# Kernel optimization log

Hardware: AMD Instinct MI355X
Metric: run time of the kernel (lower is better)

## Reference

```python
import jax, jax.numpy as jnp
import numpy as np


def _tet_geometry(vertices, indices, tet_density):
    """Gather 4 corners per tet, compute area (|det|/6), min edge length, alpha."""
    v = vertices[indices]                      # [T,4,3]
    v0, v1, v2, v3 = v[:, 0], v[:, 1], v[:, 2], v[:, 3]
    # --- tet area: |det([v1-v0, v2-v0, v3-v0])| / 6 ---
    e1, e2, e3 = v1 - v0, v2 - v0, v3 - v0     # [T,3] each
    det = (e1[:, 0] * (e2[:, 1] * e3[:, 2] - e2[:, 2] * e3[:, 1])
           - e1[:, 1] * (e2[:, 0] * e3[:, 2] - e2[:, 2] * e3[:, 0])
           + e1[:, 2] * (e2[:, 0] * e3[:, 1] - e2[:, 1] * e3[:, 0]))
    tet_area = jnp.abs(det) / 6.0              # [T]
    # --- edge lengths of all 6 edges, take min (mode='min') ---
    edge_sq = jnp.stack([
        jnp.sum((v0 - v1) ** 2, axis=1),
        jnp.sum((v0 - v2) ** 2, axis=1),
        jnp.sum((v0 - v3) ** 2, axis=1),
        jnp.sum((v1 - v2) ** 2, axis=1),
        jnp.sum((v1 - v3) ** 2, axis=1),
        jnp.sum((v2 - v3) ** 2, axis=1),
    ], axis=0)                                 # [6,T]
    el = jnp.sqrt(jnp.min(edge_sq, axis=0))    # [T]
    tet_alpha = 1.0 - jnp.exp(-tet_density * el)
    return tet_area, tet_alpha


def _vert_density(tet_density, indices, num_verts):
    # torch scatter_reduce_ 'amax' with zero-initialized dest and include_self=True
    # == segment_max over all 4 corner slots, clamped below at 0.
    flat_idx = indices.reshape(-1)                         # [4T]
    src = jnp.repeat(tet_density, 4)                       # [4T], matches row-major flatten
    vmax = jax.ops.segment_max(src, flat_idx, num_segments=num_verts)
    return jnp.maximum(vmax, jnp.zeros((), vmax.dtype))    # untouched verts -> 0


def setup_inputs() -> dict:
    key = jax.random.key(0)
    k1, k2, k3 = jax.random.split(key, 3)
    V, T = 1_000_000, 4_000_000
    vertices = jax.random.normal(k1, (V, 3), dtype=jnp.float32)
    indices = jax.random.randint(k2, (T, 4), 0, V, dtype=jnp.int32)
    tet_density = jax.random.uniform(k3, (T,), dtype=jnp.float32)
    return {"vertices": vertices, "indices": indices, "tet_density": tet_density}


def reference(vertices, indices, tet_density):
    tet_area, tet_alpha = _tet_geometry(vertices, indices, tet_density)
    vert_density = _vert_density(tet_density, indices, vertices.shape[0])
    return tet_area, tet_alpha, vert_density
```

## Files before the change

### kernel.cpp

```cpp
#include <hip/hip_runtime.h>

typedef int nt_int4 __attribute__((ext_vector_type(4)));

#define NB     256
#define VSHIFT 12
#define BMASK  ((1 << VSHIFT) - 1)
#define BCAP   65536
#define RT     2
#define NR     4

__global__ __launch_bounds__(256) void setup_kernel(uint4* __restrict__ vd4, int n4,
                                                    unsigned* __restrict__ gcnt,
                                                    const float* __restrict__ verts,
                                                    float4* __restrict__ verts4, int V) {
    int i = blockIdx.x * blockDim.x + threadIdx.x;
    if (i < n4) vd4[i] = make_uint4(0u, 0u, 0u, 0u);
    if (gcnt && i < NB) gcnt[i] = 0u;
    if (verts4 && i < V) {
        const float* p = verts + (size_t)i * 3;
        verts4[i] = make_float4(p[0], p[1], p[2], 0.f);
    }
}

__global__ __launch_bounds__(256) void fused_geom_bin_kernel(
    const float4* __restrict__ verts4,
    const int4*  __restrict__ idx4,
    const float* __restrict__ dens,
    float* __restrict__ out_area,
    float* __restrict__ out_alpha,
    uint2*       __restrict__ pairs,
    unsigned*    __restrict__ gcnt,
    unsigned*    __restrict__ vd,
    int T)
{
    __shared__ unsigned s_cnt[NB];
    __shared__ unsigned s_run[NB];
    __shared__ unsigned s_roff[NB];
    __shared__ unsigned s_wc[NB];
    __shared__ unsigned s_wsum[4];
    __shared__ uint2    stage[256 * RT * 4];

    int tid  = threadIdx.x;
    int lane = tid & 63;
    int wid  = tid >> 6;
    int base = blockIdx.x * (256 * RT * NR);

    s_cnt[tid] = 0u;
    __syncthreads();
    for (int k = 0; k < RT * NR; ++k) {
        int i = base + k * 256 + tid;
        if (i < T) {
            int4 q = idx4[i];
            atomicAdd(&s_cnt[(unsigned)q.x >> VSHIFT], 1u);
            atomicAdd(&s_cnt[(unsigned)q.y >> VSHIFT], 1u);
            atomicAdd(&s_cnt[(unsigned)q.z >> VSHIFT], 1u);
            atomicAdd(&s_cnt[(unsigned)q.w >> VSHIFT], 1u);
        }
    }
    __syncthreads();

    s_run[tid] = atomicAdd(&gcnt[tid], s_cnt[tid]);
    __syncthreads();

    int4  q[RT], qn[RT];
    float dd[RT], ddn[RT];
    bool  vl[RT], vln[RT];
    float4 pv[RT][4];

#pragma unroll
    for (int k = 0; k < RT; ++k) {
        int i = base + k * 256 + tid;
        vl[k] = (i < T);
        if (vl[k]) { q[k] = idx4[i]; dd[k] = dens[i]; }
    }
#pragma unroll
    for (int k = 0; k < RT; ++k) if (vl[k]) {
        pv[k][0] = verts4[q[k].x];
        pv[k][1] = verts4[q[k].y];
        pv[k][2] = verts4[q[k].z];
        pv[k][3] = verts4[q[k].w];
    }

    for (int r = 0; r < NR; ++r) {
        if (r + 1 < NR) {
#pragma unroll
            for (int k = 0; k < RT; ++k) {
                int i = base + ((r + 1) * RT + k) * 256 + tid;
                vln[k] = (i < T);
                if (vln[k]) { qn[k] = idx4[i]; ddn[k] = dens[i]; }
            }
        }

#pragma unroll
        for (int k = 0; k < RT; ++k) if (vl[k]) {
            int i = base + (r * RT + k) * 256 + tid;
            float4 v0 = pv[k][0], v1 = pv[k][1], v2 = pv[k][2], v3 = pv[k][3];

            float e1x = v1.x - v0.x, e1y = v1.y - v0.y, e1z = v1.z - v0.z;
            float e2x = v2.x - v0.x, e2y = v2.y - v0.y, e2z = v2.z - v0.z;
            float e3x = v3.x - v0.x, e3y = v3.y - v0.y, e3z = v3.z - v0.z;

            float det = e1x * (e2y * e3z - e2z * e3y)
                      - e1y * (e2x * e3z - e2z * e3x)
                      + e1z * (e2x * e3y - e2y * e3x);
            __builtin_nontemporal_store(fabsf(det) * (1.0f / 6.0f), &out_area[i]);

            float q01 = e1x * e1x + e1y * e1y + e1z * e1z;
            float q02 = e2x * e2x + e2y * e2y + e2z * e2z;
            float q03 = e3x * e3x + e3y * e3y + e3z * e3z;
            float ax, ay, az;
            ax = v1.x - v2.x; ay = v1.y - v2.y; az = v1.z - v2.z;
            float q12 = ax * ax + ay * ay + az * az;
            ax = v1.x - v3.x; ay = v1.y - v3.y; az = v1.z - v3.z;
            float q13 = ax * ax + ay * ay + az * az;
            ax = v2.x - v3.x; ay = v2.y - v3.y; az = v2.z - v3.z;
            float q23 = ax * ax + ay * ay + az * az;

            float mn = fminf(fminf(fminf(q01, q02), fminf(q03, q12)), fminf(q13, q23));
            float el = sqrtf(mn);
            __builtin_nontemporal_store(1.0f - expf(-dd[k] * el), &out_alpha[i]);
        }

        s_cnt[tid] = 0u;
        __syncthreads();
#pragma unroll
        for (int k = 0; k < RT; ++k) if (vl[k]) {
            atomicAdd(&s_cnt[(unsigned)q[k].x >> VSHIFT], 1u);
            atomicAdd(&s_cnt[(unsigned)q[k].y >> VSHIFT], 1u);
            atomicAdd(&s_cnt[(unsigned)q[k].z >> VSHIFT], 1u);
            atomicAdd(&s_cnt[(unsigned)q[k].w >> VSHIFT], 1u);
        }
        __syncthreads();

        unsigned x = s_cnt[tid];
        unsigned incl = x;
#pragma unroll
        for (int s = 1; s < 64; s <<= 1) {
            unsigned t = __shfl_up(incl, s);
            if (lane >= s) incl += t;
        }
        if (lane == 63) s_wsum[wid] = incl;
        __syncthreads();
        unsigned pre = 0;
#pragma unroll
        for (int w = 0; w < 4; ++w) pre += (w < wid) ? s_wsum[w] : 0u;
        unsigned npairs = s_wsum[0] + s_wsum[1] + s_wsum[2] + s_wsum[3];
        s_roff[tid] = pre + incl - x;
        s_wc[tid]   = 0u;
        __syncthreads();

        if (r + 1 < NR) {
#pragma unroll
            for (int k = 0; k < RT; ++k) if (vln[k]) {
                pv[k][0] = verts4[qn[k].x];
                pv[k][1] = verts4[qn[k].y];
                pv[k][2] = verts4[qn[k].z];
                pv[k][3] = verts4[qn[k].w];
            }
        }

#pragma unroll
        for (int k = 0; k < RT; ++k) if (vl[k]) {
            unsigned db = __float_as_uint(dd[k]);
            unsigned vv[4] = { (unsigned)q[k].x, (unsigned)q[k].y,
                               (unsigned)q[k].z, (unsigned)q[k].w };
#pragma unroll
            for (int j = 0; j < 4; ++j) {
                unsigned b    = vv[j] >> VSHIFT;
                unsigned slot = s_roff[b] + atomicAdd(&s_wc[b], 1u);
                stage[slot] = make_uint2(vv[j], db);
            }
        }
        __syncthreads();

        for (unsigned l = tid; l < npairs; l += 256) {
            uint2 e = stage[l];
            unsigned b  = e.x >> VSHIFT;
            unsigned rr = s_run[b] + (l - s_roff[b]);
            if (rr < BCAP) pairs[(size_t)b * BCAP + rr] = e;
            else           atomicMax(vd + e.x, e.y);
        }
        __syncthreads();

        s_run[tid] += s_cnt[tid];
#pragma unroll
        for (int k = 0; k < RT; ++k) { q[k] = qn[k]; dd[k] = ddn[k]; vl[k] = vln[k]; }
    }
}

__global__ __launch_bounds__(1024) void bucket_max_kernel(
    const uint2*    __restrict__ pairs,
    const unsigned* __restrict__ gcnt,
    unsigned*       __restrict__ vd,
    int V)
{
    __shared__ unsigned tbl[1 << VSHIFT];
    int b   = blockIdx.x;
    int tid = threadIdx.x;

    for (int j = tid; j < (1 << VSHIFT); j += 1024) tbl[j] = 0u;
    __syncthreads();

    unsigned cnt = gcnt[b];
    if (cnt > BCAP) cnt = BCAP;
    const uint2* p = pairs + (size_t)b * BCAP;
    for (unsigned i = tid; i < cnt; i += 1024) {
        uint2 e = p[i];
        atomicMax(&tbl[e.x & BMASK], e.y);
    }
    __syncthreads();

    int vbase = b << VSHIFT;
    for (int j = tid; j < (1 << VSHIFT); j += 1024) {
        int v = vbase + j;
        if (v < V) {
            unsigned cur = vd[v];
            unsigned t   = tbl[j];
            vd[v] = cur > t ? cur : t;
        }
    }
}

__global__ __launch_bounds__(256) void tet_kernel_filter(
    const float4* __restrict__ verts4,
    const int*   __restrict__ indices,
    const float* __restrict__ density,
    float* __restrict__ out_area,
    float* __restrict__ out_alpha,
    unsigned int* __restrict__ vd,
    int T)
{
    int i = blockIdx.x * blockDim.x + threadIdx.x;
    if (i >= T) return;

    nt_int4 idx = __builtin_nontemporal_load((const nt_int4*)indices + i);
    float d     = __builtin_nontemporal_load(&density[i]);
    unsigned int db = __float_as_uint(d);

    unsigned int c0 = vd[idx.x];
    unsigned int c1 = vd[idx.y];
    unsigned int c2 = vd[idx.z];
    unsigned int c3 = vd[idx.w];

    float4 v0 = verts4[idx.x];
    float4 v1 = verts4[idx.y];
    float4 v2 = verts4[idx.z];
    float4 v3 = verts4[idx.w];

    float e1x = v1.x - v0.x, e1y = v1.y - v0.y, e1z = v1.z - v0.z;
    float e2x = v2.x - v0.x, e2y = v2.y - v0.y, e2z = v2.z - v0.z;
    float e3x = v3.x - v0.x, e3y = v3.y - v0.y, e3z = v3.z - v0.z;

    float det = e1x * (e2y * e3z - e2z * e3y)
              - e1y * (e2x * e3z - e2z * e3x)
              + e1z * (e2x * e3y - e2y * e3x);
    __builtin_nontemporal_store(fabsf(det) * (1.0f / 6.0f), &out_area[i]);

    float q01 = e1x * e1x + e1y * e1y + e1z * e1z;
    float q02 = e2x * e2x + e2y * e2y + e2z * e2z;
    float q03 = e3x * e3x + e3y * e3y + e3z * e3z;
    float ax, ay, az;
    ax = v1.x - v2.x; ay = v1.y - v2.y; az = v1.z - v2.z;
    float q12 = ax * ax + ay * ay + az * az;
    ax = v1.x - v3.x; ay = v1.y - v3.y; az = v1.z - v3.z;
    float q13 = ax * ax + ay * ay + az * az;
    ax = v2.x - v3.x; ay = v2.y - v3.y; az = v2.z - v3.z;
    float q23 = ax * ax + ay * ay + az * az;

    float mn = fminf(fminf(fminf(q01, q02), fminf(q03, q12)), fminf(q13, q23));
    float el = sqrtf(mn);
    __builtin_nontemporal_store(1.0f - expf(-d * el), &out_alpha[i]);

    if (db > c0) atomicMax(vd + idx.x, db);
    if (db > c1) atomicMax(vd + idx.y, db);
    if (db > c2) atomicMax(vd + idx.z, db);
    if (db > c3) atomicMax(vd + idx.w, db);
}

__global__ __launch_bounds__(256) void tet_kernel_fb(
    const float* __restrict__ verts,
    const int4*  __restrict__ indices,
    const float* __restrict__ density,
    float* __restrict__ out_area,
    float* __restrict__ out_alpha,
    unsigned int* __restrict__ vd,
    int T)
{
    int i = blockIdx.x * blockDim.x + threadIdx.x;
    if (i >= T) return;

    int4 idx = indices[i];
    float d = density[i];

    const float* p;
    p = verts + idx.x * 3; float v0x = p[0], v0y = p[1], v0z = p[2];
    p = verts + idx.y * 3; float v1x = p[0], v1y = p[1], v1z = p[2];
    p = verts + idx.z * 3; float v2x = p[0], v2y = p[1], v2z = p[2];
    p = verts + idx.w * 3; float v3x = p[0], v3y = p[1], v3z = p[2];

    float e1x = v1x - v0x, e1y = v1y - v0y, e1z = v1z - v0z;
    float e2x = v2x - v0x, e2y = v2y - v0y, e2z = v2z - v0z;
    float e3x = v3x - v0x, e3y = v3y - v0y, e3z = v3z - v0z;

    float det = e1x * (e2y * e3z - e2z * e3y)
              - e1y * (e2x * e3z - e2z * e3x)
              + e1z * (e2x * e3y - e2y * e3x);
    out_area[i] = fabsf(det) * (1.0f / 6.0f);

    float q01 = e1x * e1x + e1y * e1y + e1z * e1z;
    float q02 = e2x * e2x + e2y * e2y + e2z * e2z;
    float q03 = e3x * e3x + e3y * e3y + e3z * e3z;
    float ax, ay, az;
    ax = v1x - v2x; ay = v1y - v2y; az = v1z - v2z;
    float q12 = ax * ax + ay * ay + az * az;
    ax = v1x - v3x; ay = v1y - v3y; az = v1z - v3z;
    float q13 = ax * ax + ay * ay + az * az;
    ax = v2x - v3x; ay = v2y - v3y; az = v2z - v3z;
    float q23 = ax * ax + ay * ay + az * az;

    float mn = fminf(fminf(fminf(q01, q02), fminf(q03, q12)), fminf(q13, q23));
    float el = sqrtf(mn);
    out_alpha[i] = 1.0f - expf(-d * el);

    unsigned int db = __float_as_uint(d);
    atomicMax(vd + idx.x, db);
    atomicMax(vd + idx.y, db);
    atomicMax(vd + idx.z, db);
    atomicMax(vd + idx.w, db);
}


extern "C" void kernel_launch(void* const* d_in, const int* in_sizes, int n_in,
                              void* d_out, int out_size, void* d_ws, size_t ws_size,
                              hipStream_t stream) {
    const float* verts   = (const float*)d_in[0];
    const int*   indices = (const int*)d_in[1];
    const float* density = (const float*)d_in[2];
    int T = in_sizes[2];
    int V = in_sizes[0] / 3;

    float* out       = (float*)d_out;
    float* out_area  = out;
    float* out_alpha = out + (size_t)T;
    unsigned int* vd = (unsigned int*)(out + 2 * (size_t)T);

    const int block = 256;
    int n4 = V / 4;

    size_t pairsB = (size_t)NB * BCAP * sizeof(uint2);
    size_t cntB   = (size_t)NB * sizeof(unsigned);
    size_t v4B    = (size_t)V * sizeof(float4);

    double mean = 4.0 * (double)T / NB;
    bool capOK = (mean + 12.0 * __builtin_sqrt(mean) <= (double)BCAP);
    bool fastOK = (V % 4 == 0) && (V <= (NB << VSHIFT)) && capOK && d_ws;

    int tetsPerBlock = block * RT * NR;
    int nbAct = (V + (1 << VSHIFT) - 1) >> VSHIFT;

    if (fastOK && ws_size >= pairsB + cntB + v4B) {
        uint2*    pairs  = (uint2*)d_ws;
        unsigned* gcnt   = (unsigned*)((char*)d_ws + pairsB);
        float4*   verts4 = (float4*)((char*)d_ws + pairsB + ((cntB + 255) & ~(size_t)255));

        int setupN = (V > n4 ? V : n4);
        setup_kernel<<<(setupN + block - 1) / block, block, 0, stream>>>(
            (uint4*)vd, n4, gcnt, verts, verts4, V);

        fused_geom_bin_kernel<<<(T + tetsPerBlock - 1) / tetsPerBlock, block, 0, stream>>>(
            verts4, (const int4*)indices, density, out_area, out_alpha, pairs, gcnt, vd, T);

        bucket_max_kernel<<<nbAct, 1024, 0, stream>>>(pairs, gcnt, vd, V);
    } else if (d_ws && ws_size >= v4B && (V % 4) == 0) {
        float4* verts4 = (float4*)d_ws;
        int setupN = (V > n4 ? V : n4);
        setup_kernel<<<(setupN + block - 1) / block, block, 0, stream>>>(
            (uint4*)vd, n4, nullptr, verts, verts4, V);
        tet_kernel_filter<<<(T + block - 1) / block, block, 0, stream>>>(
            verts4, indices, density, out_area, out_alpha, vd, T);
    } else {
        setup_kernel<<<(n4 + block - 1) / block, block, 0, stream>>>(
            (uint4*)vd, n4, nullptr, nullptr, nullptr, 0);
        tet_kernel_fb<<<(T + block - 1) / block, block, 0, stream>>>(
            verts, (const int4*)indices, density, out_area, out_alpha, vd, T);
    }
}
```

Before: 448.5 us.

## Drop cross-round vertex prefetch, double tets per round, vectorize bucket reads

The fused kernel no longer software-pipelines the vertex gathers for the next round across the binning phase. It instead processes twice as many tets per round (RT 2→4) and gathers vertices inline. Pair writes to the bucket buffer now use nontemporal stores, and the bucket max kernel reads two pairs per 16-byte load. The intent is to cut register pressure and raise memory-level parallelism through more independent gathers per round. The risk is losing the overlap of gather latency with the scan and scatter phases, and doubling the shared staging footprint per round.

```diff
diff --git a/kernel.cpp b/kernel.cpp
--- a/kernel.cpp
+++ b/kernel.cpp
@@ -1,12 +1,13 @@
 #include <hip/hip_runtime.h>
 
-typedef int nt_int4 __attribute__((ext_vector_type(4)));
+typedef int          nt_int4  __attribute__((ext_vector_type(4)));
+typedef unsigned int nt_uint2 __attribute__((ext_vector_type(2)));
 
 #define NB     256
 #define VSHIFT 12
 #define BMASK  ((1 << VSHIFT) - 1)
 #define BCAP   65536
-#define RT     2
+#define RT     4
 #define NR     4
 
 __global__ __launch_bounds__(256) void setup_kernel(uint4* __restrict__ vd4, int n4,
@@ -62,39 +63,24 @@
     s_run[tid] = atomicAdd(&gcnt[tid], s_cnt[tid]);
     __syncthreads();
 
-    int4  q[RT], qn[RT];
-    float dd[RT], ddn[RT];
-    bool  vl[RT], vln[RT];
-    float4 pv[RT][4];
-
-#pragma unroll
-    for (int k = 0; k < RT; ++k) {
-        int i = base + k * 256 + tid;
-        vl[k] = (i < T);
-        if (vl[k]) { q[k] = idx4[i]; dd[k] = dens[i]; }
-    }
-#pragma unroll
-    for (int k = 0; k < RT; ++k) if (vl[k]) {
-        pv[k][0] = verts4[q[k].x];
-        pv[k][1] = verts4[q[k].y];
-        pv[k][2] = verts4[q[k].z];
-        pv[k][3] = verts4[q[k].w];
-    }
-
     for (int r = 0; r < NR; ++r) {
-        if (r + 1 < NR) {
-#pragma unroll
-            for (int k = 0; k < RT; ++k) {
-                int i = base + ((r + 1) * RT + k) * 256 + tid;
-                vln[k] = (i < T);
-                if (vln[k]) { qn[k] = idx4[i]; ddn[k] = dens[i]; }
-            }
+        int4  q[RT];
+        float dd[RT];
+        bool  vl[RT];
+#pragma unroll
+        for (int k = 0; k < RT; ++k) {
+            int i = base + (r * RT + k) * 256 + tid;
+            vl[k] = (i < T);
+            if (vl[k]) { q[k] = idx4[i]; dd[k] = dens[i]; }
         }
 
 #pragma unroll
         for (int k = 0; k < RT; ++k) if (vl[k]) {
             int i = base + (r * RT + k) * 256 + tid;
-            float4 v0 = pv[k][0], v1 = pv[k][1], v2 = pv[k][2], v3 = pv[k][3];
+            float4 v0 = verts4[q[k].x];
+            float4 v1 = verts4[q[k].y];
+            float4 v2 = verts4[q[k].z];
+            float4 v3 = verts4[q[k].w];
 
             float e1x = v1.x - v0.x, e1y = v1.y - v0.y, e1z = v1.z - v0.z;
             float e2x = v2.x - v0.x, e2y = v2.y - v0.y, e2z = v2.z - v0.z;
@@ -149,16 +135,6 @@
         s_wc[tid]   = 0u;
         __syncthreads();
 
-        if (r + 1 < NR) {
-#pragma unroll
-            for (int k = 0; k < RT; ++k) if (vln[k]) {
-                pv[k][0] = verts4[qn[k].x];
-                pv[k][1] = verts4[qn[k].y];
-                pv[k][2] = verts4[qn[k].z];
-                pv[k][3] = verts4[qn[k].w];
-            }
-        }
-
 #pragma unroll
         for (int k = 0; k < RT; ++k) if (vl[k]) {
             unsigned db = __float_as_uint(dd[k]);
@@ -177,14 +153,16 @@
             uint2 e = stage[l];
             unsigned b  = e.x >> VSHIFT;
             unsigned rr = s_run[b] + (l - s_roff[b]);
-            if (rr < BCAP) pairs[(size_t)b * BCAP + rr] = e;
-            else           atomicMax(vd + e.x, e.y);
+            if (rr < BCAP) {
+                nt_uint2 ev; ev.x = e.x; ev.y = e.y;
+                __builtin_nontemporal_store(ev, (nt_uint2*)(pairs + (size_t)b * BCAP + rr));
+            } else {
+                atomicMax(vd + e.x, e.y);
+            }
         }
         __syncthreads();
 
         s_run[tid] += s_cnt[tid];
-#pragma unroll
-        for (int k = 0; k < RT; ++k) { q[k] = qn[k]; dd[k] = ddn[k]; vl[k] = vln[k]; }
     }
 }
 
@@ -203,9 +181,15 @@
 
     unsigned cnt = gcnt[b];
     if (cnt > BCAP) cnt = BCAP;
-    const uint2* p = pairs + (size_t)b * BCAP;
-    for (unsigned i = tid; i < cnt; i += 1024) {
-        uint2 e = p[i];
+    const uint4* p4 = (const uint4*)(pairs + (size_t)b * BCAP);
+    unsigned n2 = cnt >> 1;
+    for (unsigned i = tid; i < n2; i += 1024) {
+        uint4 e = p4[i];
+        atomicMax(&tbl[e.x & BMASK], e.y);
+        atomicMax(&tbl[e.z & BMASK], e.w);
+    }
+    if (tid == 0 && (cnt & 1u)) {
+        uint2 e = pairs[(size_t)b * BCAP + cnt - 1];
         atomicMax(&tbl[e.x & BMASK], e.y);
     }
     __syncthreads();
```

After: 434.1 us. 3.2% less time.
